# Kernel tuning notes

Measured on AMD Instinct MI355X. Metric: run time of the kernel, lower is better.

Reference implementation:

```python
import math
import jax, jax.numpy as jnp
import numpy as np

B, T, C = 2, 2048, 1024
N_HEAD = 16
HEAD_DIM = C // N_HEAD


def setup_inputs() -> dict:
    key = jax.random.key(0)
    k1, k2, k3 = jax.random.split(key, 3)
    std = 0.02
    return {
        "x": jax.random.normal(k1, (B, T, C), dtype=jnp.float32),
        "W_qkv": jax.random.normal(k2, (3 * C, C), dtype=jnp.float32) * std,
        "b_qkv": jnp.zeros((3 * C,), dtype=jnp.float32),
        "W_proj": jax.random.normal(k3, (C, C), dtype=jnp.float32) * std,
        "b_proj": jnp.zeros((C,), dtype=jnp.float32),
    }


def reference(x, W_qkv, b_qkv, W_proj, b_proj):
    Bs, Ts, Cs = x.shape
    # qkv projection, split as [3][n_head][head_dim] along last dim (matches torch view order)
    qkv = (x @ W_qkv.T + b_qkv).reshape(Bs, Ts, 3, N_HEAD, HEAD_DIM)
    qkv = qkv.transpose(0, 3, 2, 1, 4)  # (B, H, 3, T, hd)
    q, k, v = qkv[:, :, 0], qkv[:, :, 1], qkv[:, :, 2]  # each (B, H, T, hd)
    scale = 1.0 / math.sqrt(HEAD_DIM)
    att = jnp.einsum('bhtd,bhsd->bhts', q, k) * scale  # (B, H, T, T)
    causal = jnp.tril(jnp.ones((Ts, Ts), dtype=bool))
    att = jnp.where(causal, att, -jnp.inf)
    att = jax.nn.softmax(att, axis=-1)
    y = jnp.einsum('bhts,bhsd->bhtd', att, v)  # (B, H, T, hd)
    y = y.transpose(0, 2, 1, 3).reshape(Bs, Ts, Cs)
    return y @ W_proj.T + b_proj
```

## Files before the change

### kernel.cpp

```cpp
#include <hip/hip_runtime.h>
#include <cstdint>

#define BDIM  2
#define TSEQ  2048
#define CDIM  1024
#define NHEAD 16
#define HDIM  64
#define C3    3072

typedef __attribute__((ext_vector_type(8))) short short8_t;
typedef __attribute__((ext_vector_type(4))) short short4_t;
typedef __attribute__((ext_vector_type(4))) float f32x4;

static __device__ __forceinline__ unsigned short f2bf(float f) {
  union { float f; unsigned u; } v; v.f = f;
  unsigned r = v.u + 0x7FFFu + ((v.u >> 16) & 1u);
  return (unsigned short)(r >> 16);
}
static __device__ __forceinline__ unsigned cvtpk_bf16(float lo, float hi) {
  unsigned r;
  asm("v_cvt_pk_bf16_f32 %0, %1, %2" : "=v"(r) : "v"(lo), "v"(hi));
  return r;
}
static __device__ __forceinline__ void g2lds16(const unsigned short* g,
                                               unsigned short* l) {
  __builtin_amdgcn_global_load_lds(
      (const __attribute__((address_space(1))) void*)g,
      (__attribute__((address_space(3))) void*)l, 16, 0, 0);
}
static __device__ __forceinline__ void bar_lds() {
  asm volatile("s_waitcnt lgkmcnt(0)\n\ts_barrier" ::: "memory");
}

__device__ __forceinline__ int kk_idx(int row, int chunk) {
  return row * 64 + (((chunk ^ (row & 7)) & 7) << 3);
}
__device__ __forceinline__ int vv_idx(int d, int chunk) {
  return d * 64 + (((chunk ^ (d & 7) ^ ((d >> 3) & 7)) & 7) << 3);
}

__global__ __launch_bounds__(256) void f32_to_bf16_3(
    const float* __restrict__ x, const float* __restrict__ wq,
    const float* __restrict__ wp, unsigned short* __restrict__ outb,
    int n1, int n2, int n3)
{
  const int i = blockIdx.x * 256 + threadIdx.x;
  const float* src; unsigned short* dst; int j;
  if (i < n1)            { src = x;  dst = outb;                        j = i; }
  else if (i < n1 + n2)  { src = wq; dst = outb + (size_t)n1 * 4;       j = i - n1; }
  else if (i < n1+n2+n3) { src = wp; dst = outb + (size_t)(n1+n2) * 4;  j = i - n1 - n2; }
  else return;
  const float4 v = ((const float4*)src)[j];
  const unsigned lo = (unsigned)f2bf(v.x) | ((unsigned)f2bf(v.y) << 16);
  const unsigned hi = (unsigned)f2bf(v.z) | ((unsigned)f2bf(v.w) << 16);
  ((uint2*)dst)[j] = make_uint2(lo, hi);
}

template <int FJ, bool OUT_BF16, int MWPE>
__global__ __launch_bounds__(256, MWPE) void gemm_bt_mfma(
    const unsigned short* __restrict__ A, const unsigned short* __restrict__ B,
    const float* __restrict__ bias, void* __restrict__ Cv,
    int M, int N, int K)
{
  __shared__ unsigned short As[128 * 64];
  __shared__ unsigned short Bs[FJ * 32 * 64];

  const int tid  = threadIdx.x;
  const int lane = tid & 63;
  const int wv   = tid >> 6;
  const int wr   = wv >> 1, wc = wv & 1;
  const int l15  = lane & 15, g = lane >> 4;
  const int bn = blockIdx.x, bm = blockIdx.y;

  const int srow = tid >> 3;
  const int chg  = (tid & 7) ^ (srow & 7);
  const unsigned short* Ab = A + (size_t)(bm * 128 + srow) * K + chg * 8;
  const unsigned short* Bb = B + (size_t)(bn * (FJ * 32) + srow) * K + chg * 8;

  f32x4 acc[4][FJ];
#pragma unroll
  for (int i = 0; i < 4; ++i)
#pragma unroll
    for (int j = 0; j < FJ; ++j) acc[i][j] = (f32x4){0.f, 0.f, 0.f, 0.f};

  for (int k0 = 0; k0 < K; k0 += 64) {
    __syncthreads();
#pragma unroll
    for (int c = 0; c < 4; ++c)
      g2lds16(Ab + (size_t)(c * 32) * K + k0, &As[c * 2048 + wv * 512]);
#pragma unroll
    for (int c = 0; c < FJ; ++c)
      g2lds16(Bb + (size_t)(c * 32) * K + k0, &Bs[c * 2048 + wv * 512]);
    __syncthreads();

#pragma unroll
    for (int kk = 0; kk < 2; ++kk) {
      short8_t af[4], bf[FJ];
#pragma unroll
      for (int i = 0; i < 4; ++i)
        af[i] = *(const short8_t*)&As[kk_idx(wr * 64 + i * 16 + l15, kk * 4 + g)];
#pragma unroll
      for (int j = 0; j < FJ; ++j)
        bf[j] = *(const short8_t*)&Bs[kk_idx(wc * (FJ * 16) + j * 16 + l15, kk * 4 + g)];
#pragma unroll
      for (int i = 0; i < 4; ++i)
#pragma unroll
        for (int j = 0; j < FJ; ++j)
          acc[i][j] = __builtin_amdgcn_mfma_f32_16x16x32_bf16(af[i], bf[j], acc[i][j], 0, 0, 0);
    }
  }

#pragma unroll
  for (int j = 0; j < FJ; ++j) {
    const int col = bn * (FJ * 32) + wc * (FJ * 16) + j * 16 + l15;
    const float bj = bias[col];
#pragma unroll
    for (int i = 0; i < 4; ++i) {
#pragma unroll
      for (int r = 0; r < 4; ++r) {
        const int row = bm * 128 + wr * 64 + i * 16 + g * 4 + r;
        const float v = acc[i][j][r] + bj;
        if (OUT_BF16) ((unsigned short*)Cv)[(size_t)row * N + col] = f2bf(v);
        else          ((float*)Cv)[(size_t)row * N + col] = v;
      }
    }
  }
}

__global__ __launch_bounds__(512, 8) void attn_mfma(
    const unsigned short* __restrict__ qkv, unsigned short* __restrict__ yb)
{
  __shared__ unsigned short SM[37888];
  unsigned short* Ks = SM;
  unsigned short* Vt = SM + 16384;
  unsigned short* Ps = SM + 32768;

  const int tid  = threadIdx.x;
  const int lane = tid & 63;
  const int wv   = tid >> 6;
  const int qs   = wv & 3;
  const int kvh  = wv >> 2;
  const int l15  = lane & 15, g = lane >> 4;

  const int nfl = blockIdx.x;
  const int x   = (nfl >> 3) & 15;
  const int grp = (nfl & 7) | ((nfl >> 7) << 3);
  const int h = grp & 15, b = grp >> 4;

  const unsigned short* kbase = qkv + (size_t)(b * TSEQ) * C3 + CDIM + h * HDIM;
  const unsigned short* vbase = kbase + CDIM;
  unsigned short* Pw = &Ps[wv * 640];

  const float SC2 = 0.18033688011112042f;
  const float THR = 11.5415603f;

  const int skv = tid >> 3, sc = tid & 7;
  const int kwo = kk_idx(skv, sc);
  const int vs = tid >> 4, dh = (tid >> 3) & 1, va = tid & 7;
  int vwo[4];
#pragma unroll
  for (int j = 0; j < 4; ++j)
    vwo[j] = vv_idx(va * 8 + dh * 4 + j, vs >> 2) + ((2 * vs) & 7);

  for (int ph = 0; ph < 2; ++ph) {
    const int qt   = ph ? (31 - x) : x;
    const int wq0  = qt * 64 + qs * 16;
    const int q_hi = wq0 + 15;
    const int qg   = wq0 + l15;
    const int fastc = qt >> 1;

    short8_t qf[2];
#pragma unroll
    for (int kk = 0; kk < 2; ++kk)
      qf[kk] = *(const short8_t*)(qkv +
          (size_t)(b * TSEQ + wq0 + l15) * C3 + h * HDIM + kk * 32 + g * 8);

    f32x4 O[4];
#pragma unroll
    for (int n = 0; n < 4; ++n) O[n] = (f32x4){0.f, 0.f, 0.f, 0.f};
    float Mr = 0.0f, Lr = 0.f;

    const unsigned short* kptr  = kbase + (size_t)skv * C3 + sc * 8;
    const unsigned short* vptr0 = vbase + (size_t)(2 * vs) * C3 + va * 8 + dh * 4;
    short8_t pk0 = *(const short8_t*)(kptr);
    short8_t pk1 = *(const short8_t*)(kptr + (size_t)64 * C3);
    short4_t pv0 = *(const short4_t*)(vptr0);
    short4_t pv1 = *(const short4_t*)(vptr0 + C3);
    short4_t pv2 = *(const short4_t*)(vptr0 + (size_t)64 * C3);
    short4_t pv3 = *(const short4_t*)(vptr0 + (size_t)65 * C3);

    for (int c = 0; c < fastc; ++c) {
      const int p2 = (c & 1) << 1;
      {
        unsigned short* K0 = &Ks[p2 * 4096];
        unsigned short* K1 = &Ks[(p2 + 1) * 4096];
        unsigned short* V0 = &Vt[p2 * 4096];
        unsigned short* V1 = &Vt[(p2 + 1) * 4096];
        *(short8_t*)&K0[kwo] = pk0;
        *(short8_t*)&K1[kwo] = pk1;
        const unsigned short* e0 = (const unsigned short*)&pv0;
        const unsigned short* e1 = (const unsigned short*)&pv1;
        const unsigned short* e2 = (const unsigned short*)&pv2;
        const unsigned short* e3 = (const unsigned short*)&pv3;
#pragma unroll
        for (int j = 0; j < 4; ++j) {
          *(unsigned*)&V0[vwo[j]] = (unsigned)e0[j] | ((unsigned)e1[j] << 16);
          *(unsigned*)&V1[vwo[j]] = (unsigned)e2[j] | ((unsigned)e3[j] << 16);
        }
      }
      bar_lds();
      kptr  += (size_t)128 * C3;
      vptr0 += (size_t)128 * C3;
      pk0 = *(const short8_t*)(kptr);
      pk1 = *(const short8_t*)(kptr + (size_t)64 * C3);
      pv0 = *(const short4_t*)(vptr0);
      pv1 = *(const short4_t*)(vptr0 + C3);
      pv2 = *(const short4_t*)(vptr0 + (size_t)64 * C3);
      pv3 = *(const short4_t*)(vptr0 + (size_t)65 * C3);

#pragma unroll
      for (int sub = 0; sub < 2; ++sub) {
        const unsigned short* Kc = &Ks[(p2 + sub) * 4096];
        const unsigned short* Vc = &Vt[(p2 + sub) * 4096];

        f32x4 s[2];
#pragma unroll
        for (int n = 0; n < 2; ++n) s[n] = (f32x4){0.f, 0.f, 0.f, 0.f};
        __builtin_amdgcn_s_setprio(1);
#pragma unroll
        for (int n = 0; n < 2; ++n) {
#pragma unroll
          for (int kk = 0; kk < 2; ++kk) {
            const short8_t kf =
                *(const short8_t*)&Kc[kk_idx(kvh * 32 + n * 16 + l15, kk * 4 + g)];
            s[n] = __builtin_amdgcn_mfma_f32_16x16x32_bf16(kf, qf[kk], s[n], 0, 0, 0);
          }
        }
        __builtin_amdgcn_s_setprio(0);

        float mt = -3.0e38f, rs = 0.f;
#pragma unroll
        for (int n = 0; n < 2; ++n)
#pragma unroll
          for (int r = 0; r < 4; ++r) mt = fmaxf(mt, s[n][r]);
#pragma unroll
        for (int n = 0; n < 2; ++n)
#pragma unroll
          for (int r = 0; r < 4; ++r) {
            const float p = __builtin_amdgcn_exp2f(fmaf(s[n][r], SC2, -Mr));
            s[n][r] = p;
            rs += p;
          }
        Lr += rs;
#pragma unroll
        for (int n = 0; n < 2; ++n) {
          const unsigned u0 = cvtpk_bf16(s[n][0], s[n][1]);
          const unsigned u1 = cvtpk_bf16(s[n][2], s[n][3]);
          *(uint2*)&Pw[l15 * 40 + n * 16 + (g << 2)] = make_uint2(u0, u1);
        }
        mt *= SC2;
        if (__any(mt > Mr + THR)) {
          mt = fmaxf(mt, __shfl_xor(mt, 16));
          mt = fmaxf(mt, __shfl_xor(mt, 32));
          const float nm = fmaxf(Mr, mt);
          const float al = __builtin_amdgcn_exp2f(Mr - nm);
          Lr *= al;
          float alq[4];
#pragma unroll
          for (int r = 0; r < 4; ++r) alq[r] = __shfl(al, (g << 2) + r);
#pragma unroll
          for (int n = 0; n < 4; ++n)
#pragma unroll
            for (int r = 0; r < 4; ++r) O[n][r] *= alq[r];
          Mr = nm;
#pragma unroll
          for (int n = 0; n < 2; ++n) {
#pragma unroll
            for (int r = 0; r < 4; ++r) s[n][r] *= al;
            const unsigned u0 = cvtpk_bf16(s[n][0], s[n][1]);
            const unsigned u1 = cvtpk_bf16(s[n][2], s[n][3]);
            *(uint2*)&Pw[l15 * 40 + n * 16 + (g << 2)] = make_uint2(u0, u1);
          }
        }

        const short8_t pf = *(const short8_t*)&Pw[l15 * 40 + g * 8];
        __builtin_amdgcn_s_setprio(1);
#pragma unroll
        for (int n = 0; n < 4; ++n) {
          const short8_t vf = *(const short8_t*)&Vc[vv_idx(n * 16 + l15, kvh * 4 + g)];
          O[n] = __builtin_amdgcn_mfma_f32_16x16x32_bf16(pf, vf, O[n], 0, 0, 0);
        }
        __builtin_amdgcn_s_setprio(0);
      }
    }

    {
      const int p2 = (fastc & 1) << 1;
      {
        unsigned short* K0 = &Ks[p2 * 4096];
        unsigned short* K1 = &Ks[(p2 + 1) * 4096];
        unsigned short* V0 = &Vt[p2 * 4096];
        unsigned short* V1 = &Vt[(p2 + 1) * 4096];
        *(short8_t*)&K0[kwo] = pk0;
        *(short8_t*)&K1[kwo] = pk1;
        const unsigned short* e0 = (const unsigned short*)&pv0;
        const unsigned short* e1 = (const unsigned short*)&pv1;
        const unsigned short* e2 = (const unsigned short*)&pv2;
        const unsigned short* e3 = (const unsigned short*)&pv3;
#pragma unroll
        for (int j = 0; j < 4; ++j) {
          *(unsigned*)&V0[vwo[j]] = (unsigned)e0[j] | ((unsigned)e1[j] << 16);
          *(unsigned*)&V1[vwo[j]] = (unsigned)e2[j] | ((unsigned)e3[j] << 16);
        }
      }
      bar_lds();

#pragma unroll
      for (int sub = 0; sub < 2; ++sub) {
        const int kvw0 = fastc * 128 + sub * 64 + kvh * 32;
        if (kvw0 > q_hi) continue;
        const unsigned short* Kc = &Ks[(p2 + sub) * 4096];
        const unsigned short* Vc = &Vt[(p2 + sub) * 4096];
        const int nl = (q_hi - kvw0) >> 4;
        const int nlim = (nl > 1) ? 1 : nl;

        f32x4 s[2];
#pragma unroll
        for (int n = 0; n < 2; ++n) s[n] = (f32x4){0.f, 0.f, 0.f, 0.f};
        __builtin_amdgcn_s_setprio(1);
#pragma unroll
        for (int n = 0; n < 2; ++n) {
          if (n <= nlim) {
#pragma unroll
            for (int kk = 0; kk < 2; ++kk) {
              const short8_t kf =
                  *(const short8_t*)&Kc[kk_idx(kvh * 32 + n * 16 + l15, kk * 4 + g)];
              s[n] = __builtin_amdgcn_mfma_f32_16x16x32_bf16(kf, qf[kk], s[n], 0, 0, 0);
            }
          }
        }
        __builtin_amdgcn_s_setprio(0);

        float mt = -3.0e38f;
#pragma unroll
        for (int n = 0; n < 2; ++n) {
          if (n <= nlim) {
            const int kvb = kvw0 + n * 16 + g * 4;
            const bool needmask = (kvw0 + n * 16 + 15 > wq0);
#pragma unroll
            for (int r = 0; r < 4; ++r) {
              float v = s[n][r] * SC2;
              if (needmask && (kvb + r > qg)) v = -3.0e38f;
              s[n][r] = v;
              mt = fmaxf(mt, v);
            }
          }
        }
        float rs = 0.f;
#pragma unroll
        for (int n = 0; n < 2; ++n) {
          if (n <= nlim) {
#pragma unroll
            for (int r = 0; r < 4; ++r) {
              const float p = __builtin_amdgcn_exp2f(s[n][r] - Mr);
              s[n][r] = p;
              rs += p;
            }
          }
        }
        Lr += rs;
#pragma unroll
        for (int n = 0; n < 2; ++n) {
          const unsigned u0 = cvtpk_bf16(s[n][0], s[n][1]);
          const unsigned u1 = cvtpk_bf16(s[n][2], s[n][3]);
          *(uint2*)&Pw[l15 * 40 + n * 16 + (g << 2)] = make_uint2(u0, u1);
        }
        if (__any(mt > Mr + THR)) {
          mt = fmaxf(mt, __shfl_xor(mt, 16));
          mt = fmaxf(mt, __shfl_xor(mt, 32));
          const float nm = fmaxf(Mr, mt);
          const float al = __builtin_amdgcn_exp2f(Mr - nm);
          Lr *= al;
          float alq[4];
#pragma unroll
          for (int r = 0; r < 4; ++r) alq[r] = __shfl(al, (g << 2) + r);
#pragma unroll
          for (int n = 0; n < 4; ++n)
#pragma unroll
            for (int r = 0; r < 4; ++r) O[n][r] *= alq[r];
          Mr = nm;
#pragma unroll
          for (int n = 0; n < 2; ++n) {
            if (n <= nlim) {
#pragma unroll
              for (int r = 0; r < 4; ++r) s[n][r] *= al;
            }
            const unsigned u0 = cvtpk_bf16(s[n][0], s[n][1]);
            const unsigned u1 = cvtpk_bf16(s[n][2], s[n][3]);
            *(uint2*)&Pw[l15 * 40 + n * 16 + (g << 2)] = make_uint2(u0, u1);
          }
        }

        const short8_t pf = *(const short8_t*)&Pw[l15 * 40 + g * 8];
        __builtin_amdgcn_s_setprio(1);
#pragma unroll
        for (int n = 0; n < 4; ++n) {
          const short8_t vf = *(const short8_t*)&Vc[vv_idx(n * 16 + l15, kvh * 4 + g)];
          O[n] = __builtin_amdgcn_mfma_f32_16x16x32_bf16(pf, vf, O[n], 0, 0, 0);
        }
        __builtin_amdgcn_s_setprio(0);
      }
    }

    Lr += __shfl_xor(Lr, 16);
    Lr += __shfl_xor(Lr, 32);

    __syncthreads();
    {
      float* Cb = (float*)SM;
      const int slot = (qs * 64 + lane) * 18;
      if (kvh == 1) {
#pragma unroll
        for (int n = 0; n < 4; ++n)
#pragma unroll
          for (int r = 0; r < 4; ++r) Cb[slot + n * 4 + r] = O[n][r];
        Cb[slot + 16] = Mr;
        Cb[slot + 17] = Lr;
      }
    }
    __syncthreads();
    if (kvh == 0) {
      const float* Cb = (const float*)SM;
      const int slot = (qs * 64 + lane) * 18;
      const float m2 = Cb[slot + 16], l2 = Cb[slot + 17];
      const float m  = fmaxf(Mr, m2);
      const float a1 = __builtin_amdgcn_exp2f(Mr - m);
      const float a2 = __builtin_amdgcn_exp2f(m2 - m);
      const float inv = 1.0f / (Lr * a1 + l2 * a2);
      const float fa = a1 * inv, fb = a2 * inv;
      float faq[4], fbq[4];
#pragma unroll
      for (int r = 0; r < 4; ++r) {
        faq[r] = __shfl(fa, (g << 2) + r);
        fbq[r] = __shfl(fb, (g << 2) + r);
      }
#pragma unroll
      for (int n = 0; n < 4; ++n)
#pragma unroll
        for (int r = 0; r < 4; ++r) {
          const float o2 = Cb[slot + n * 4 + r];
          const size_t row = (size_t)(b * TSEQ + wq0 + (g << 2) + r);
          yb[row * CDIM + h * HDIM + n * 16 + l15] =
              f2bf(O[n][r] * faq[r] + o2 * fbq[r]);
        }
    }
    __syncthreads();
  }
}

extern "C" void kernel_launch(void* const* d_in, const int* in_sizes, int n_in,
                              void* d_out, int out_size, void* d_ws, size_t ws_size,
                              hipStream_t stream)
{
  const float* x     = (const float*)d_in[0];
  const float* Wqkv  = (const float*)d_in[1];
  const float* bqkv  = (const float*)d_in[2];
  const float* Wproj = (const float*)d_in[3];
  const float* bproj = (const float*)d_in[4];
  float* out = (float*)d_out;

  const int M = BDIM * TSEQ;
  unsigned short* qkv = (unsigned short*)d_ws;
  unsigned short* yb  = qkv + (size_t)M * C3;
  unsigned short* xb  = yb  + (size_t)M * CDIM;
  unsigned short* wqb = xb  + (size_t)M * CDIM;
  unsigned short* wpb = wqb + (size_t)C3 * CDIM;

  const int n1 = M * CDIM / 4, n2 = C3 * CDIM / 4, n3 = CDIM * CDIM / 4;
  f32_to_bf16_3<<<(n1 + n2 + n3 + 255) / 256, 256, 0, stream>>>(
      x, Wqkv, Wproj, xb, n1, n2, n3);

  gemm_bt_mfma<4, true, 3><<<dim3(C3 / 128, M / 128), 256, 0, stream>>>(
      xb, wqb, bqkv, (void*)qkv, M, C3, CDIM);

  attn_mfma<<<dim3(512, 1, 1), 512, 0, stream>>>(qkv, yb);

  gemm_bt_mfma<2, false, 2><<<dim3(CDIM / 64, M / 128), 256, 0, stream>>>(
      yb, wpb, bproj, (void*)out, M, CDIM, CDIM);
}
```

Before: 92.79 us.

## Permute K rows so softmax P stays in registers as MFMA operand

Reorders which K rows each lane loads so that the S accumulator layout from the QK^T MFMA directly matches the A-operand layout needed by the PV MFMA. The P tile no longer goes through an LDS store and reload, and the P scratch region of shared memory is removed. The diagonal-block path drops its partial-tile skipping and always computes both 16-column subtiles, masking per element, which trades a little extra MFMA work for simpler code.

```diff
diff --git a/kernel.cpp b/kernel.cpp
--- a/kernel.cpp
+++ b/kernel.cpp
@@ -130,10 +130,9 @@
 __global__ __launch_bounds__(512, 8) void attn_mfma(
     const unsigned short* __restrict__ qkv, unsigned short* __restrict__ yb)
 {
-  __shared__ unsigned short SM[37888];
+  __shared__ unsigned short SM[32768];
   unsigned short* Ks = SM;
   unsigned short* Vt = SM + 16384;
-  unsigned short* Ps = SM + 32768;
 
   const int tid  = threadIdx.x;
   const int lane = tid & 63;
@@ -141,6 +140,7 @@
   const int qs   = wv & 3;
   const int kvh  = wv >> 2;
   const int l15  = lane & 15, g = lane >> 4;
+  const int sig  = 8 * (l15 >> 2) + (l15 & 3);
 
   const int nfl = blockIdx.x;
   const int x   = (nfl >> 3) & 15;
@@ -149,7 +149,6 @@
 
   const unsigned short* kbase = qkv + (size_t)(b * TSEQ) * C3 + CDIM + h * HDIM;
   const unsigned short* vbase = kbase + CDIM;
-  unsigned short* Pw = &Ps[wv * 640];
 
   const float SC2 = 0.18033688011112042f;
   const float THR = 11.5415603f;
@@ -232,7 +231,7 @@
 #pragma unroll
           for (int kk = 0; kk < 2; ++kk) {
             const short8_t kf =
-                *(const short8_t*)&Kc[kk_idx(kvh * 32 + n * 16 + l15, kk * 4 + g)];
+                *(const short8_t*)&Kc[kk_idx(kvh * 32 + sig + n * 4, kk * 4 + g)];
             s[n] = __builtin_amdgcn_mfma_f32_16x16x32_bf16(kf, qf[kk], s[n], 0, 0, 0);
           }
         }
@@ -252,12 +251,11 @@
             rs += p;
           }
         Lr += rs;
-#pragma unroll
-        for (int n = 0; n < 2; ++n) {
-          const unsigned u0 = cvtpk_bf16(s[n][0], s[n][1]);
-          const unsigned u1 = cvtpk_bf16(s[n][2], s[n][3]);
-          *(uint2*)&Pw[l15 * 40 + n * 16 + (g << 2)] = make_uint2(u0, u1);
-        }
+        uint4 pu;
+        pu.x = cvtpk_bf16(s[0][0], s[0][1]);
+        pu.y = cvtpk_bf16(s[0][2], s[0][3]);
+        pu.z = cvtpk_bf16(s[1][0], s[1][1]);
+        pu.w = cvtpk_bf16(s[1][2], s[1][3]);
         mt *= SC2;
         if (__any(mt > Mr + THR)) {
           mt = fmaxf(mt, __shfl_xor(mt, 16));
@@ -274,16 +272,16 @@
             for (int r = 0; r < 4; ++r) O[n][r] *= alq[r];
           Mr = nm;
 #pragma unroll
-          for (int n = 0; n < 2; ++n) {
+          for (int n = 0; n < 2; ++n)
 #pragma unroll
             for (int r = 0; r < 4; ++r) s[n][r] *= al;
-            const unsigned u0 = cvtpk_bf16(s[n][0], s[n][1]);
-            const unsigned u1 = cvtpk_bf16(s[n][2], s[n][3]);
-            *(uint2*)&Pw[l15 * 40 + n * 16 + (g << 2)] = make_uint2(u0, u1);
-          }
-        }
-
-        const short8_t pf = *(const short8_t*)&Pw[l15 * 40 + g * 8];
+          pu.x = cvtpk_bf16(s[0][0], s[0][1]);
+          pu.y = cvtpk_bf16(s[0][2], s[0][3]);
+          pu.z = cvtpk_bf16(s[1][0], s[1][1]);
+          pu.w = cvtpk_bf16(s[1][2], s[1][3]);
+        }
+        const short8_t pf = *(const short8_t*)&pu;
+
         __builtin_amdgcn_s_setprio(1);
 #pragma unroll
         for (int n = 0; n < 4; ++n) {
@@ -321,8 +319,6 @@
         if (kvw0 > q_hi) continue;
         const unsigned short* Kc = &Ks[(p2 + sub) * 4096];
         const unsigned short* Vc = &Vt[(p2 + sub) * 4096];
-        const int nl = (q_hi - kvw0) >> 4;
-        const int nlim = (nl > 1) ? 1 : nl;
 
         f32x4 s[2];
 #pragma unroll
@@ -330,51 +326,41 @@
         __builtin_amdgcn_s_setprio(1);
 #pragma unroll
         for (int n = 0; n < 2; ++n) {
-          if (n <= nlim) {
-#pragma unroll
-            for (int kk = 0; kk < 2; ++kk) {
-              const short8_t kf =
-                  *(const short8_t*)&Kc[kk_idx(kvh * 32 + n * 16 + l15, kk * 4 + g)];
-              s[n] = __builtin_amdgcn_mfma_f32_16x16x32_bf16(kf, qf[kk], s[n], 0, 0, 0);
-            }
+#pragma unroll
+          for (int kk = 0; kk < 2; ++kk) {
+            const short8_t kf =
+                *(const short8_t*)&Kc[kk_idx(kvh * 32 + sig + n * 4, kk * 4 + g)];
+            s[n] = __builtin_amdgcn_mfma_f32_16x16x32_bf16(kf, qf[kk], s[n], 0, 0, 0);
           }
         }
         __builtin_amdgcn_s_setprio(0);
 
-        float mt = -3.0e38f;
+        float mt = -3.0e38f, rs = 0.f;
 #pragma unroll
         for (int n = 0; n < 2; ++n) {
-          if (n <= nlim) {
-            const int kvb = kvw0 + n * 16 + g * 4;
-            const bool needmask = (kvw0 + n * 16 + 15 > wq0);
-#pragma unroll
-            for (int r = 0; r < 4; ++r) {
-              float v = s[n][r] * SC2;
-              if (needmask && (kvb + r > qg)) v = -3.0e38f;
-              s[n][r] = v;
-              mt = fmaxf(mt, v);
-            }
+          const int kvb = kvw0 + 8 * g + n * 4;
+#pragma unroll
+          for (int r = 0; r < 4; ++r) {
+            float v = s[n][r] * SC2;
+            if (kvb + r > qg) v = -3.0e38f;
+            s[n][r] = v;
+            mt = fmaxf(mt, v);
           }
         }
-        float rs = 0.f;
-#pragma unroll
-        for (int n = 0; n < 2; ++n) {
-          if (n <= nlim) {
-#pragma unroll
-            for (int r = 0; r < 4; ++r) {
-              const float p = __builtin_amdgcn_exp2f(s[n][r] - Mr);
-              s[n][r] = p;
-              rs += p;
-            }
+#pragma unroll
+        for (int n = 0; n < 2; ++n)
+#pragma unroll
+          for (int r = 0; r < 4; ++r) {
+            const float p = __builtin_amdgcn_exp2f(s[n][r] - Mr);
+            s[n][r] = p;
+            rs += p;
           }
-        }
         Lr += rs;
-#pragma unroll
-        for (int n = 0; n < 2; ++n) {
-          const unsigned u0 = cvtpk_bf16(s[n][0], s[n][1]);
-          const unsigned u1 = cvtpk_bf16(s[n][2], s[n][3]);
-          *(uint2*)&Pw[l15 * 40 + n * 16 + (g << 2)] = make_uint2(u0, u1);
-        }
+        uint4 pu;
+        pu.x = cvtpk_bf16(s[0][0], s[0][1]);
+        pu.y = cvtpk_bf16(s[0][2], s[0][3]);
+        pu.z = cvtpk_bf16(s[1][0], s[1][1]);
+        pu.w = cvtpk_bf16(s[1][2], s[1][3]);
         if (__any(mt > Mr + THR)) {
           mt = fmaxf(mt, __shfl_xor(mt, 16));
           mt = fmaxf(mt, __shfl_xor(mt, 32));
@@ -390,18 +376,16 @@
             for (int r = 0; r < 4; ++r) O[n][r] *= alq[r];
           Mr = nm;
 #pragma unroll
-          for (int n = 0; n < 2; ++n) {
-            if (n <= nlim) {
-#pragma unroll
-              for (int r = 0; r < 4; ++r) s[n][r] *= al;
-            }
-            const unsigned u0 = cvtpk_bf16(s[n][0], s[n][1]);
-            const unsigned u1 = cvtpk_bf16(s[n][2], s[n][3]);
-            *(uint2*)&Pw[l15 * 40 + n * 16 + (g << 2)] = make_uint2(u0, u1);
-          }
-        }
-
-        const short8_t pf = *(const short8_t*)&Pw[l15 * 40 + g * 8];
+          for (int n = 0; n < 2; ++n)
+#pragma unroll
+            for (int r = 0; r < 4; ++r) s[n][r] *= al;
+          pu.x = cvtpk_bf16(s[0][0], s[0][1]);
+          pu.y = cvtpk_bf16(s[0][2], s[0][3]);
+          pu.z = cvtpk_bf16(s[1][0], s[1][1]);
+          pu.w = cvtpk_bf16(s[1][2], s[1][3]);
+        }
+        const short8_t pf = *(const short8_t*)&pu;
+
         __builtin_amdgcn_s_setprio(1);
 #pragma unroll
         for (int n = 0; n < 4; ++n) {
```

Measured after the change: 90.03 us, median of 2. 3.0% less time.
